# Performance work log

Measured on AMD Instinct MI355X. Metric: run time of the kernel, lower is better.

Reference implementation:

```python
import jax, jax.numpy as jnp
import numpy as np
from jax import lax

DIM = 128  # per-head dim used for scaling


def setup_inputs() -> dict:
    key = jax.random.key(0)
    ks = jax.random.split(key, 6)
    B, S, D = 16, 2048, DIM
    query = jax.random.normal(ks[0], (B, S, D), dtype=jnp.float32)
    k = jax.random.normal(ks[1], (B, S, D), dtype=jnp.float32)
    value = jax.random.normal(ks[2], (B, S, D), dtype=jnp.float32)
    mask = jax.random.randint(ks[3], (B, 1, S), 0, 2, dtype=jnp.int32)
    conv_w = jax.random.normal(ks[4], (B, 1, 3, 3), dtype=jnp.float32) * 0.1  # depthwise 3x3, OIHW
    conv_b = jax.random.normal(ks[5], (B,), dtype=jnp.float32) * 0.1
    return {"query": query, "key": k, "value": value, "mask": mask,
            "conv_w": conv_w, "conv_b": conv_b}


def reference(query, key, value, mask, conv_w, conv_b):
    B = query.shape[0]
    # score: (B, Sq, Sk)
    score = jnp.einsum('bqd,bkd->bqk', query, key) / jnp.float32(np.sqrt(DIM))
    # depthwise 3x3 conv over the score map; score treated as (C=B, H=Sq, W=Sk)
    conv = lax.conv_general_dilated(
        score[None],                      # (1, B, Sq, Sk)
        conv_w,                           # (B, 1, 3, 3)
        window_strides=(1, 1), padding='SAME',
        feature_group_count=B,
        dimension_numbers=('NCHW', 'OIHW', 'NCHW'))[0]
    conv = jax.nn.relu(conv + conv_b[:, None, None])
    conv_score = score + conv
    conv_score = jnp.where(mask == 0, jnp.float32(-1e9), conv_score)
    atten = jax.nn.softmax(conv_score, axis=-1)  # attn_drop=0.0 -> identity
    context = jnp.einsum('bqk,bkd->bqd', atten, value)
    return (context, atten)
```

## Files before the change

### kernel.cpp

```cpp
#include <hip/hip_runtime.h>
#include <stdint.h>

#define B_BATCH 16
#define SEQ     2048
#define DIMD    128
#define QT_OUT  14
#define SROWS   16
#define TILES_PB 147
#define SCALE   0.08838834764831845f
#define L2E     1.4426950408889634f

#define SC_STRIDE 4096
#define LDS_TOTAL (SROWS * SC_STRIDE)

typedef __attribute__((ext_vector_type(8))) short bf16x8;
typedef __attribute__((ext_vector_type(4))) float f32x4;

__device__ __forceinline__ unsigned short f2bf(float f) {
  union { float f; uint32_t u; } v; v.f = f;
  uint32_t u = v.u;
  return (unsigned short)((u + 0x7FFFu + ((u >> 16) & 1u)) >> 16);
}
__device__ __forceinline__ float bf2f(unsigned short h) {
  union { uint32_t u; float f; } v; v.u = ((uint32_t)h) << 16;
  return v.f;
}

__global__ __launch_bounds__(256) void cvt_bf16(const float* __restrict__ in,
                                                unsigned short* __restrict__ out) {
  const size_t i = (size_t)blockIdx.x * 256 + threadIdx.x;
  const float4 a = *(const float4*)(in + i * 8);
  const float4 b = *(const float4*)(in + i * 8 + 4);
  uint4 o;
  o.x = (uint32_t)f2bf(a.x) | ((uint32_t)f2bf(a.y) << 16);
  o.y = (uint32_t)f2bf(a.z) | ((uint32_t)f2bf(a.w) << 16);
  o.z = (uint32_t)f2bf(b.x) | ((uint32_t)f2bf(b.y) << 16);
  o.w = (uint32_t)f2bf(b.z) | ((uint32_t)f2bf(b.w) << 16);
  *(uint4*)(out + i * 8) = o;
}

__global__ __launch_bounds__(256) void transpose_v(const float* __restrict__ V,
                                                   unsigned short* __restrict__ Vt) {
  __shared__ float tl[64][65];
  const int b  = blockIdx.x >> 6;
  const int kt = (blockIdx.x & 63) >> 1;
  const int dt = blockIdx.x & 1;
  const int k0 = kt * 64, d0 = dt * 64;
  const int tid = threadIdx.x;
  const int r = tid >> 4, c4 = (tid & 15) * 4;
  const float* Vb = V + (size_t)b * SEQ * DIMD;
#pragma unroll
  for (int ii = 0; ii < 4; ++ii) {
    const int row = ii * 16 + r;
    float4 v = *(const float4*)(Vb + (size_t)(k0 + row) * DIMD + d0 + c4);
    tl[row][c4 + 0] = v.x; tl[row][c4 + 1] = v.y;
    tl[row][c4 + 2] = v.z; tl[row][c4 + 3] = v.w;
  }
  __syncthreads();
  unsigned short* VtB = Vt + (size_t)b * DIMD * SEQ;
#pragma unroll
  for (int ii = 0; ii < 4; ++ii) {
    const int drow = ii * 16 + r;
    ushort4 o;
    o.x = f2bf(tl[c4 + 0][drow]); o.y = f2bf(tl[c4 + 1][drow]);
    o.z = f2bf(tl[c4 + 2][drow]); o.w = f2bf(tl[c4 + 3][drow]);
    *(ushort4*)(VtB + (size_t)(d0 + drow) * SEQ + k0 + c4) = o;
  }
}

__global__ __launch_bounds__(512, 4) void fused_attn(
    const float* __restrict__ Q, const unsigned short* __restrict__ Kb,
    const unsigned short* __restrict__ Vt, const int* __restrict__ msk,
    const float* __restrict__ cw, const float* __restrict__ cbv,
    float* __restrict__ ctx, float* __restrict__ attn) {
  __shared__ __align__(16) char smem[LDS_TOTAL];

  const int bid = blockIdx.x;
  const int b  = bid & 15;
  const int t  = bid >> 4;
  const int g0 = t * QT_OUT;
  const int tid = threadIdx.x;
  const int w = tid >> 6, lane = tid & 63, l15 = lane & 15, hi = lane >> 4;

  float w9[9];
#pragma unroll
  for (int i = 0; i < 9; ++i) w9[i] = cw[b * 9 + i];
  const float bias = cbv[b];

  uint32_t mb = 0;
  {
    const int* mp = msk + b * SEQ;
#pragma unroll
    for (int jb = 0; jb < 4; ++jb) {
      int4 a = *(const int4*)(mp + jb * 512 + lane * 8);
      int4 bq = *(const int4*)(mp + jb * 512 + lane * 8 + 4);
      mb |= (a.x  != 0 ? 1u : 0u) << (jb * 8 + 0);
      mb |= (a.y  != 0 ? 1u : 0u) << (jb * 8 + 1);
      mb |= (a.z  != 0 ? 1u : 0u) << (jb * 8 + 2);
      mb |= (a.w  != 0 ? 1u : 0u) << (jb * 8 + 3);
      mb |= (bq.x != 0 ? 1u : 0u) << (jb * 8 + 4);
      mb |= (bq.y != 0 ? 1u : 0u) << (jb * 8 + 5);
      mb |= (bq.z != 0 ? 1u : 0u) << (jb * 8 + 6);
      mb |= (bq.w != 0 ? 1u : 0u) << (jb * 8 + 7);
    }
  }

  bf16x8 aq[4];
  {
    int grow = g0 - 1 + l15;
    grow = grow < 0 ? 0 : (grow > SEQ - 1 ? SEQ - 1 : grow);
    const float* qp = Q + ((size_t)(b * SEQ + grow)) * DIMD + hi * 8;
#pragma unroll
    for (int ks = 0; ks < 4; ++ks) {
      float4 x = *(const float4*)(qp + ks * 32);
      float4 y = *(const float4*)(qp + ks * 32 + 4);
      bf16x8 f;
      f[0] = (short)f2bf(x.x); f[1] = (short)f2bf(x.y);
      f[2] = (short)f2bf(x.z); f[3] = (short)f2bf(x.w);
      f[4] = (short)f2bf(y.x); f[5] = (short)f2bf(y.y);
      f[6] = (short)f2bf(y.z); f[7] = (short)f2bf(y.w);
      aq[ks] = f;
    }
  }

  {
    const unsigned short* KbB = Kb + (size_t)b * SEQ * DIMD;
    const int k0w = w * 256;
#pragma unroll 4
    for (int kc = 0; kc < 16; ++kc) {
      const int k0 = k0w + kc * 16;
      const unsigned short* kp = KbB + (size_t)(k0 + l15) * DIMD + hi * 8;
      bf16x8 bk0 = *(const bf16x8*)(kp);
      bf16x8 bk1 = *(const bf16x8*)(kp + 32);
      bf16x8 bk2 = *(const bf16x8*)(kp + 64);
      bf16x8 bk3 = *(const bf16x8*)(kp + 96);
      f32x4 acc = {0.f, 0.f, 0.f, 0.f};
      acc = __builtin_amdgcn_mfma_f32_16x16x32_bf16(aq[0], bk0, acc, 0, 0, 0);
      acc = __builtin_amdgcn_mfma_f32_16x16x32_bf16(aq[1], bk1, acc, 0, 0, 0);
      acc = __builtin_amdgcn_mfma_f32_16x16x32_bf16(aq[2], bk2, acc, 0, 0, 0);
      acc = __builtin_amdgcn_mfma_f32_16x16x32_bf16(aq[3], bk3, acc, 0, 0, 0);
      const int colb = (k0 + l15) * 2;
#pragma unroll
      for (int r = 0; r < 4; ++r) {
        const int row = hi * 4 + r;
        *(unsigned short*)(smem + row * SC_STRIDE + (colb ^ ((row & 7) << 4))) =
            f2bf(acc[r] * SCALE);
      }
    }
  }
  __syncthreads();

  const int nrows = (SEQ - g0) < QT_OUT ? (SEQ - g0) : QT_OUT;

  for (int sp = 0; sp < 2; ++sp) {
    const int i = sp * 8 + w;
    const bool act = (i < nrows);
    float p[32];
    float inv = 0.f;
    if (act) {
      const int g = g0 + i;
      const bool vtop = (g > 0), vbot = (g + 1 < SEQ);
#pragma unroll
      for (int jb = 0; jb < 4; ++jb) {
        float m[3][8], Lv[3], Rv[3];
#pragma unroll
        for (int r = 0; r < 3; ++r) {
          const bool v = (r == 1) || ((r == 0) ? vtop : vbot);
          if (v) {
            const int row = i + r;
            const int rs = row * SC_STRIDE, sw = (row & 7) << 4;
            bf16x8 vv = *(const bf16x8*)(smem + rs + ((jb * 1024 + lane * 16) ^ sw));
#pragma unroll
            for (int c = 0; c < 8; ++c) m[r][c] = bf2f((unsigned short)vv[c]);
            float le = 0.f, re = 0.f;
            if (jb > 0)
              le = bf2f(*(const unsigned short*)(smem + rs + (((jb * 512 - 1) * 2) ^ sw)));
            if (jb < 3)
              re = bf2f(*(const unsigned short*)(smem + rs + (((jb * 512 + 512) * 2) ^ sw)));
            const float lsh = __shfl_up(m[r][7], 1);
            const float rsh = __shfl_down(m[r][0], 1);
            Lv[r] = (lane == 0)  ? le : lsh;
            Rv[r] = (lane == 63) ? re : rsh;
          } else {
#pragma unroll
            for (int c = 0; c < 8; ++c) m[r][c] = 0.f;
            Lv[r] = 0.f; Rv[r] = 0.f;
          }
        }
#pragma unroll
        for (int c = 0; c < 8; ++c) {
          float cv = 0.f;
#pragma unroll
          for (int r = 0; r < 3; ++r) {
            const float lft = (c == 0) ? Lv[r] : m[r][c - 1];
            const float rgt = (c == 7) ? Rv[r] : m[r][c + 1];
            cv += w9[r * 3 + 0] * lft + w9[r * 3 + 1] * m[r][c] + w9[r * 3 + 2] * rgt;
          }
          const float val = m[1][c] + fmaxf(cv + bias, 0.f);
          p[jb * 8 + c] = ((mb >> (jb * 8 + c)) & 1u) ? val : -1e9f;
        }
      }
      float mx = p[0];
#pragma unroll
      for (int k = 1; k < 32; ++k) mx = fmaxf(mx, p[k]);
#pragma unroll
      for (int o = 1; o < 64; o <<= 1) mx = fmaxf(mx, __shfl_xor(mx, o, 64));
      float Z = 0.f;
#pragma unroll
      for (int k = 0; k < 32; ++k) {
        p[k] = __builtin_amdgcn_exp2f((p[k] - mx) * L2E);
        Z += p[k];
      }
#pragma unroll
      for (int o = 1; o < 64; o <<= 1) Z += __shfl_xor(Z, o, 64);
      inv = 1.0f / Z;
    }
    __syncthreads();
    if (act) {
      const int rs = i * SC_STRIDE, sw = (i & 7) << 4;
#pragma unroll
      for (int jb = 0; jb < 4; ++jb) {
        bf16x8 h;
#pragma unroll
        for (int c = 0; c < 8; ++c) h[c] = (short)f2bf(p[jb * 8 + c] * inv);
        *(bf16x8*)(smem + rs + ((jb * 1024 + lane * 16) ^ sw)) = h;
      }
    }
    __syncthreads();
  }

  {
    const unsigned short* vp =
        Vt + (size_t)b * DIMD * SEQ + (size_t)(16 * w + l15) * SEQ + hi * 8;
    const int abase = l15 * SC_STRIDE;
    const int asw = (l15 & 7) << 4;
    f32x4 acc0 = {0.f, 0.f, 0.f, 0.f}, acc1 = {0.f, 0.f, 0.f, 0.f};
#pragma unroll 4
    for (int kc = 0; kc < 32; ++kc) {
      const int k0 = kc * 64;
      bf16x8 a0 = *(const bf16x8*)(smem + abase + (((k0      ) * 2 + hi * 16) ^ asw));
      bf16x8 b0 = *(const bf16x8*)(vp + k0);
      acc0 = __builtin_amdgcn_mfma_f32_16x16x32_bf16(a0, b0, acc0, 0, 0, 0);
      bf16x8 a1 = *(const bf16x8*)(smem + abase + (((k0 + 32) * 2 + hi * 16) ^ asw));
      bf16x8 b1 = *(const bf16x8*)(vp + k0 + 32);
      acc1 = __builtin_amdgcn_mfma_f32_16x16x32_bf16(a1, b1, acc1, 0, 0, 0);
    }
    const int col = 16 * w + l15;
#pragma unroll
    for (int r = 0; r < 4; ++r) {
      const int row = hi * 4 + r;
      const int g = g0 + row;
      if (row < QT_OUT && g < SEQ)
        __builtin_nontemporal_store(acc0[r] + acc1[r],
                                    &ctx[((size_t)(b * SEQ + g)) * DIMD + col]);
    }
  }

  {
    float* attnB = attn + (size_t)b * SEQ * SEQ;
#pragma unroll
    for (int sp = 0; sp < 2; ++sp) {
      const int i = sp * 8 + w;
      if (i < nrows) {
        const int g = g0 + i;
        float* arow = attnB + (size_t)g * SEQ;
        const int rs = i * SC_STRIDE, sw = (i & 7) << 4;
#pragma unroll
        for (int jb = 0; jb < 8; ++jb) {
          uint2 hv = *(const uint2*)(smem + rs + ((jb * 512 + lane * 8) ^ sw));
          f32x4 o;
          o[0] = bf2f((unsigned short)(hv.x & 0xffffu));
          o[1] = bf2f((unsigned short)(hv.x >> 16));
          o[2] = bf2f((unsigned short)(hv.y & 0xffffu));
          o[3] = bf2f((unsigned short)(hv.y >> 16));
          __builtin_nontemporal_store(o, (f32x4*)(arow + jb * 256 + lane * 4));
        }
      }
    }
  }
}

extern "C" void kernel_launch(void* const* d_in, const int* in_sizes, int n_in,
                              void* d_out, int out_size, void* d_ws, size_t ws_size,
                              hipStream_t stream) {
  const float* Q  = (const float*)d_in[0];
  const float* K  = (const float*)d_in[1];
  const float* V  = (const float*)d_in[2];
  const int* msk  = (const int*)d_in[3];
  const float* cw = (const float*)d_in[4];
  const float* cb = (const float*)d_in[5];
  float* ctx  = (float*)d_out;
  float* attn = ctx + (size_t)B_BATCH * SEQ * DIMD;
  unsigned short* Kb = (unsigned short*)d_ws;
  unsigned short* Vt = Kb + (size_t)B_BATCH * SEQ * DIMD;

  cvt_bf16<<<2048, 256, 0, stream>>>(K, Kb);
  transpose_v<<<B_BATCH * 64, 256, 0, stream>>>(V, Vt);
  fused_attn<<<B_BATCH * TILES_PB, 512, 0, stream>>>(Q, Kb, Vt, msk, cw, cb, ctx, attn);
}
```

Before: 366.9 us.

## Split fused attention into separate QK, conv-softmax, and PV kernels

```diff
diff --git a/kernel.cpp b/kernel.cpp
--- a/kernel.cpp
+++ b/kernel.cpp
@@ -68,19 +68,68 @@
   }
 }
 
-__global__ __launch_bounds__(512, 4) void fused_attn(
-    const float* __restrict__ Q, const unsigned short* __restrict__ Kb,
-    const unsigned short* __restrict__ Vt, const int* __restrict__ msk,
-    const float* __restrict__ cw, const float* __restrict__ cbv,
-    float* __restrict__ ctx, float* __restrict__ attn) {
-  __shared__ __align__(16) char smem[LDS_TOTAL];
-
+__global__ __launch_bounds__(512, 4) void qk_gemm(
+    const unsigned short* __restrict__ Qb, const unsigned short* __restrict__ Kb,
+    unsigned short* __restrict__ S) {
+  __shared__ __align__(16) char sm[128 * 256];
   const int bid = blockIdx.x;
-  const int b  = bid & 15;
-  const int t  = bid >> 4;
-  const int g0 = t * QT_OUT;
+  const int b = bid & 15, t = bid >> 4, tr = t & 15, tc = t >> 4;
   const int tid = threadIdx.x;
   const int w = tid >> 6, lane = tid & 63, l15 = lane & 15, hi = lane >> 4;
+  const int wr = w >> 2, wc = w & 3;
+
+  const unsigned short* Qp =
+      Qb + ((size_t)(b * SEQ) + tr * 128 + wr * 64) * DIMD;
+  const unsigned short* Kp =
+      Kb + ((size_t)(b * SEQ) + tc * 128 + wc * 32) * DIMD;
+
+  f32x4 acc[4][2] = {};
+#pragma unroll
+  for (int ks = 0; ks < 4; ++ks) {
+    bf16x8 aq[4], bk[2];
+#pragma unroll
+    for (int fr = 0; fr < 4; ++fr)
+      aq[fr] = *(const bf16x8*)(Qp + (size_t)(fr * 16 + l15) * DIMD + ks * 32 + hi * 8);
+#pragma unroll
+    for (int fc = 0; fc < 2; ++fc)
+      bk[fc] = *(const bf16x8*)(Kp + (size_t)(fc * 16 + l15) * DIMD + ks * 32 + hi * 8);
+#pragma unroll
+    for (int fr = 0; fr < 4; ++fr)
+#pragma unroll
+      for (int fc = 0; fc < 2; ++fc)
+        acc[fr][fc] = __builtin_amdgcn_mfma_f32_16x16x32_bf16(aq[fr], bk[fc], acc[fr][fc], 0, 0, 0);
+  }
+#pragma unroll
+  for (int fr = 0; fr < 4; ++fr)
+#pragma unroll
+    for (int fc = 0; fc < 2; ++fc)
+#pragma unroll
+      for (int r = 0; r < 4; ++r) {
+        const int row = wr * 64 + fr * 16 + hi * 4 + r;
+        const int colb = (wc * 32 + fc * 16 + l15) * 2;
+        *(unsigned short*)(sm + row * 256 + (colb ^ ((row & 7) << 4))) =
+            f2bf(acc[fr][fc][r] * SCALE);
+      }
+  __syncthreads();
+  unsigned short* Sp = S + ((size_t)(b * SEQ) + tr * 128) * SEQ + tc * 128;
+  const int rr = tid >> 4, cc = tid & 15;
+#pragma unroll
+  for (int p = 0; p < 4; ++p) {
+    const int row = p * 32 + rr;
+    bf16x8 v = *(const bf16x8*)(sm + row * 256 + ((cc * 16) ^ ((row & 7) << 4)));
+    *(bf16x8*)(Sp + (size_t)row * SEQ + cc * 8) = v;
+  }
+}
+
+__global__ __launch_bounds__(512, 4) void conv_softmax(
+    const unsigned short* __restrict__ S, const int* __restrict__ msk,
+    const float* __restrict__ cw, const float* __restrict__ cbv,
+    float* __restrict__ attn) {
+  const int bid = blockIdx.x;
+  const int b = bid & 15, rblk = bid >> 4;
+  const int tid = threadIdx.x;
+  const int w = tid >> 6, lane = tid & 63;
+  const int g = rblk * 8 + w;
 
   float w9[9];
 #pragma unroll
@@ -105,6 +154,148 @@
     }
   }
 
+  const unsigned short* Sb = S + (size_t)b * SEQ * SEQ;
+  const bool vtop = (g > 0), vbot = (g + 1 < SEQ);
+  float p[32];
+#pragma unroll
+  for (int jb = 0; jb < 4; ++jb) {
+    float m[3][8], Lv[3], Rv[3];
+#pragma unroll
+    for (int r = 0; r < 3; ++r) {
+      const bool v = (r == 1) || ((r == 0) ? vtop : vbot);
+      if (v) {
+        const unsigned short* srow = Sb + (size_t)(g - 1 + r) * SEQ;
+        bf16x8 vv = *(const bf16x8*)(srow + jb * 512 + lane * 8);
+#pragma unroll
+        for (int c = 0; c < 8; ++c) m[r][c] = bf2f((unsigned short)vv[c]);
+        float le = 0.f, re = 0.f;
+        if (jb > 0) le = bf2f(srow[jb * 512 - 1]);
+        if (jb < 3) re = bf2f(srow[jb * 512 + 512]);
+        const float lsh = __shfl_up(m[r][7], 1);
+        const float rsh = __shfl_down(m[r][0], 1);
+        Lv[r] = (lane == 0)  ? le : lsh;
+        Rv[r] = (lane == 63) ? re : rsh;
+      } else {
+#pragma unroll
+        for (int c = 0; c < 8; ++c) m[r][c] = 0.f;
+        Lv[r] = 0.f; Rv[r] = 0.f;
+      }
+    }
+#pragma unroll
+    for (int c = 0; c < 8; ++c) {
+      float cv = 0.f;
+#pragma unroll
+      for (int r = 0; r < 3; ++r) {
+        const float lft = (c == 0) ? Lv[r] : m[r][c - 1];
+        const float rgt = (c == 7) ? Rv[r] : m[r][c + 1];
+        cv += w9[r * 3 + 0] * lft + w9[r * 3 + 1] * m[r][c] + w9[r * 3 + 2] * rgt;
+      }
+      const float val = m[1][c] + fmaxf(cv + bias, 0.f);
+      p[jb * 8 + c] = ((mb >> (jb * 8 + c)) & 1u) ? val : -1e9f;
+    }
+  }
+  float mx = p[0];
+#pragma unroll
+  for (int k = 1; k < 32; ++k) mx = fmaxf(mx, p[k]);
+#pragma unroll
+  for (int o = 1; o < 64; o <<= 1) mx = fmaxf(mx, __shfl_xor(mx, o, 64));
+  float Z = 0.f;
+#pragma unroll
+  for (int k = 0; k < 32; ++k) {
+    p[k] = __builtin_amdgcn_exp2f((p[k] - mx) * L2E);
+    Z += p[k];
+  }
+#pragma unroll
+  for (int o = 1; o < 64; o <<= 1) Z += __shfl_xor(Z, o, 64);
+  const float inv = 1.0f / Z;
+
+  float* arow = attn + (size_t)b * SEQ * SEQ + (size_t)g * SEQ;
+#pragma unroll
+  for (int jb = 0; jb < 4; ++jb) {
+    f32x4 o0, o1;
+    o0[0] = p[jb * 8 + 0] * inv; o0[1] = p[jb * 8 + 1] * inv;
+    o0[2] = p[jb * 8 + 2] * inv; o0[3] = p[jb * 8 + 3] * inv;
+    o1[0] = p[jb * 8 + 4] * inv; o1[1] = p[jb * 8 + 5] * inv;
+    o1[2] = p[jb * 8 + 6] * inv; o1[3] = p[jb * 8 + 7] * inv;
+    __builtin_nontemporal_store(o0, (f32x4*)(arow + jb * 512 + lane * 8));
+    __builtin_nontemporal_store(o1, (f32x4*)(arow + jb * 512 + lane * 8 + 4));
+  }
+}
+
+__global__ __launch_bounds__(512, 4) void pv_gemm(
+    const float* __restrict__ attn, const unsigned short* __restrict__ Vt,
+    float* __restrict__ ctx) {
+  const int bid = blockIdx.x;
+  const int b = bid & 15, rt = bid >> 4;
+  const int tid = threadIdx.x;
+  const int w = tid >> 6, lane = tid & 63, l15 = lane & 15, hi = lane >> 4;
+  const int wr = w >> 1, wc = w & 1;
+
+  const float* Ap =
+      attn + ((size_t)b * SEQ + rt * 64 + wr * 16 + l15) * SEQ + hi * 8;
+  const unsigned short* Vp = Vt + ((size_t)b * DIMD + wc * 64) * SEQ;
+
+  f32x4 acc[4] = {};
+#pragma unroll 4
+  for (int kk = 0; kk < 64; ++kk) {
+    const int k0 = kk * 32;
+    float4 x = *(const float4*)(Ap + k0);
+    float4 y = *(const float4*)(Ap + k0 + 4);
+    bf16x8 a;
+    a[0] = (short)f2bf(x.x); a[1] = (short)f2bf(x.y);
+    a[2] = (short)f2bf(x.z); a[3] = (short)f2bf(x.w);
+    a[4] = (short)f2bf(y.x); a[5] = (short)f2bf(y.y);
+    a[6] = (short)f2bf(y.z); a[7] = (short)f2bf(y.w);
+#pragma unroll
+    for (int fc = 0; fc < 4; ++fc) {
+      bf16x8 bv = *(const bf16x8*)(Vp + (size_t)(fc * 16 + l15) * SEQ + k0 + hi * 8);
+      acc[fc] = __builtin_amdgcn_mfma_f32_16x16x32_bf16(a, bv, acc[fc], 0, 0, 0);
+    }
+  }
+#pragma unroll
+  for (int fc = 0; fc < 4; ++fc)
+#pragma unroll
+    for (int r = 0; r < 4; ++r) {
+      const int row = rt * 64 + wr * 16 + hi * 4 + r;
+      const int col = wc * 64 + fc * 16 + l15;
+      ctx[((size_t)b * SEQ + row) * DIMD + col] = acc[fc][r];
+    }
+}
+
+__global__ __launch_bounds__(512, 4) void fused_attn(
+    const float* __restrict__ Q, const unsigned short* __restrict__ Kb,
+    const unsigned short* __restrict__ Vt, const int* __restrict__ msk,
+    const float* __restrict__ cw, const float* __restrict__ cbv,
+    float* __restrict__ ctx, float* __restrict__ attn) {
+  __shared__ __align__(16) char smem[LDS_TOTAL];
+  const int bid = blockIdx.x;
+  const int b  = bid & 15;
+  const int t  = bid >> 4;
+  const int g0 = t * QT_OUT;
+  const int tid = threadIdx.x;
+  const int w = tid >> 6, lane = tid & 63, l15 = lane & 15, hi = lane >> 4;
+
+  float w9[9];
+#pragma unroll
+  for (int i = 0; i < 9; ++i) w9[i] = cw[b * 9 + i];
+  const float bias = cbv[b];
+  uint32_t mb = 0;
+  {
+    const int* mp = msk + b * SEQ;
+#pragma unroll
+    for (int jb = 0; jb < 4; ++jb) {
+      int4 a = *(const int4*)(mp + jb * 512 + lane * 8);
+      int4 bq = *(const int4*)(mp + jb * 512 + lane * 8 + 4);
+      mb |= (a.x  != 0 ? 1u : 0u) << (jb * 8 + 0);
+      mb |= (a.y  != 0 ? 1u : 0u) << (jb * 8 + 1);
+      mb |= (a.z  != 0 ? 1u : 0u) << (jb * 8 + 2);
+      mb |= (a.w  != 0 ? 1u : 0u) << (jb * 8 + 3);
+      mb |= (bq.x != 0 ? 1u : 0u) << (jb * 8 + 4);
+      mb |= (bq.y != 0 ? 1u : 0u) << (jb * 8 + 5);
+      mb |= (bq.z != 0 ? 1u : 0u) << (jb * 8 + 6);
+      mb |= (bq.w != 0 ? 1u : 0u) << (jb * 8 + 7);
+    }
+  }
   bf16x8 aq[4];
   {
     int grow = g0 - 1 + l15;
@@ -122,7 +313,6 @@
       aq[ks] = f;
     }
   }
-
   {
     const unsigned short* KbB = Kb + (size_t)b * SEQ * DIMD;
     const int k0w = w * 256;
@@ -149,9 +339,7 @@
     }
   }
   __syncthreads();
-
   const int nrows = (SEQ - g0) < QT_OUT ? (SEQ - g0) : QT_OUT;
-
   for (int sp = 0; sp < 2; ++sp) {
     const int i = sp * 8 + w;
     const bool act = (i < nrows);
@@ -228,7 +416,6 @@
     }
     __syncthreads();
   }
-
   {
     const unsigned short* vp =
         Vt + (size_t)b * DIMD * SEQ + (size_t)(16 * w + l15) * SEQ + hi * 8;
@@ -251,11 +438,9 @@
       const int row = hi * 4 + r;
       const int g = g0 + row;
       if (row < QT_OUT && g < SEQ)
-        __builtin_nontemporal_store(acc0[r] + acc1[r],
-                                    &ctx[((size_t)(b * SEQ + g)) * DIMD + col]);
-    }
-  }
-
+        ctx[((size_t)(b * SEQ + g)) * DIMD + col] = acc0[r] + acc1[r];
+    }
+  }
   {
     float* attnB = attn + (size_t)b * SEQ * SEQ;
 #pragma unroll
@@ -291,10 +476,27 @@
   const float* cb = (const float*)d_in[5];
   float* ctx  = (float*)d_out;
   float* attn = ctx + (size_t)B_BATCH * SEQ * DIMD;
-  unsigned short* Kb = (unsigned short*)d_ws;
-  unsigned short* Vt = Kb + (size_t)B_BATCH * SEQ * DIMD;
-
-  cvt_bf16<<<2048, 256, 0, stream>>>(K, Kb);
-  transpose_v<<<B_BATCH * 64, 256, 0, stream>>>(V, Vt);
-  fused_attn<<<B_BATCH * TILES_PB, 512, 0, stream>>>(Q, Kb, Vt, msk, cw, cb, ctx, attn);
-}
+
+  const size_t nQK = (size_t)B_BATCH * SEQ * DIMD;
+  const size_t nS  = (size_t)B_BATCH * SEQ * SEQ;
+  const size_t need = (3 * nQK + nS) * sizeof(unsigned short);
+
+  if (ws_size >= need) {
+    unsigned short* Qb = (unsigned short*)d_ws;
+    unsigned short* Kb = Qb + nQK;
+    unsigned short* Vt = Kb + nQK;
+    unsigned short* S  = Vt + nQK;
+    cvt_bf16<<<2048, 256, 0, stream>>>(Q, Qb);
+    cvt_bf16<<<2048, 256, 0, stream>>>(K, Kb);
+    transpose_v<<<B_BATCH * 64, 256, 0, stream>>>(V, Vt);
+    qk_gemm<<<4096, 512, 0, stream>>>(Qb, Kb, S);
+    conv_softmax<<<4096, 512, 0, stream>>>(S, msk, cw, cb, attn);
+    pv_gemm<<<512, 512, 0, stream>>>(attn, Vt, ctx);
+  } else {
+    unsigned short* Kb = (unsigned short*)d_ws;
+    unsigned short* Vt = Kb + nQK;
+    cvt_bf16<<<2048, 256, 0, stream>>>(K, Kb);
+    transpose_v<<<B_BATCH * 64, 256, 0, stream>>>(V, Vt);
+    fused_attn<<<B_BATCH * TILES_PB, 512, 0, stream>>>(Q, Kb, Vt, msk, cw, cb, ctx, attn);
+  }
+}
```

Result: slower. 503.6 us (+37.3%).
